# Kernel optimization log

Hardware: AMD Instinct MI355X
Metric: run time of the kernel (lower is better)

The kernel has to match this reference:

```python
import jax, jax.numpy as jnp
import numpy as np

ALPHA = 0.5
N_CACHE = 8
N_HEAD = 16
NUM_MODULES = 4


def _ncn_module(x, xa, W, alpha, n_cache, n_head):
    """One fused NCN module: per-head mix, alpha blend with cache slot (t % n_cache),
    activation, and cache update. x: [B,T,D], xa: [B,n_cache,D], W: [H,dh,dh]."""
    B, T, D = x.shape
    dh = D // n_head
    xh = x.reshape(B, T, n_head, dh).transpose(1, 0, 2, 3)  # [T,B,H,dh]
    cache0 = xa.reshape(B, n_cache, n_head, dh)             # [B,C,H,dh]
    slots = jnp.arange(T) % n_cache                          # cache slot per step

    def step(cache, inp):
        xt, s = inp                                          # xt: [B,H,dh]
        mix = jnp.einsum('bhd,hde->bhe', xt, W)              # per-head mixing
        y = jnp.tanh(alpha * cache[:, s] + (1.0 - alpha) * mix)
        return cache.at[:, s].set(y), y

    cache_f, ys = jax.lax.scan(step, cache0, (xh, slots))
    yi = ys.transpose(1, 0, 2, 3).reshape(B, T, D)
    ya = cache_f.reshape(B, n_cache, D)
    return yi, ya


def setup_inputs() -> dict:
    key = jax.random.key(0)
    k1, k2, k3 = jax.random.split(key, 3)
    B, T, D = 8, 4096, 1024
    dh = D // N_HEAD
    x = jax.random.normal(k1, (B, T, D), dtype=jnp.float32)
    xa = jax.random.normal(k2, (B, N_CACHE, D), dtype=jnp.float32)
    # scale weights for stable tanh recurrence
    weights = jax.random.normal(k3, (NUM_MODULES, N_HEAD, dh, dh), dtype=jnp.float32) / np.sqrt(dh)
    return {"x": x, "xa": xa, "weights": weights}


def reference(x, xa, weights):
    for m in range(NUM_MODULES):
        x, xa = _ncn_module(x, xa, weights[m], ALPHA, N_CACHE, N_HEAD)
    return x, xa
```

## Files before the change

kernel.cpp:

```cpp
#include <hip/hip_runtime.h>
#include <hip/hip_fp16.h>


typedef _Float16 f16;
typedef _Float16 half8 __attribute__((ext_vector_type(8)));
typedef _Float16 half4v __attribute__((ext_vector_type(4)));
typedef float f32x4 __attribute__((ext_vector_type(4)));
typedef unsigned uint4v __attribute__((ext_vector_type(4)));

constexpr int B = 8, T = 4096, D = 1024, H = 16, DH = 64, NC = 8, NM = 4;
constexpr int CH = 256;
constexpr int NCHUNK = T / CH;
constexpr int RPC = 128;

__global__ __launch_bounds__(256, 1)
void ncn_main(const float* __restrict__ x, const float* __restrict__ xa,
              const float* __restrict__ w, float* __restrict__ out) {
  __shared__ __align__(16) unsigned char YL[RPC * 128];
  __shared__ __align__(16) unsigned char MX[64 * 256];

  const int tid = threadIdx.x, lane = tid & 63, wv = tid >> 6;
  const int bx = blockIdx.x;
  const int chalf = bx & 1, h = (bx >> 1) & 15, b = bx >> 5;
  const int cbase = chalf * 4;
  const int lr = lane & 15, lg = lane >> 4;
  const int c = cbase + wv;
  const int d = lane;

  unsigned char* const rows = (unsigned char*)out + (size_t)b * T * 4096;
  const unsigned char* const xrows =
      (const unsigned char*)x + (size_t)b * T * 4096;

  float cache = xa[((size_t)b * NC + c) * D + h * DH + d];

  uint4v pf[8];

  for (int m = 0; m < NM; ++m) {
    const float* wh = w + ((size_t)m * H + h) * DH * DH;
    half8 Wf[4][2];
#pragma unroll
    for (int it = 0; it < 4; ++it)
#pragma unroll
      for (int kt = 0; kt < 2; ++kt)
#pragma unroll
        for (int j = 0; j < 8; ++j)
          Wf[it][kt][j] =
              (f16)wh[(size_t)(kt * 32 + lg * 8 + j) * DH + it * 16 + lr];

    asm volatile("s_waitcnt vmcnt(0)" ::: "memory");
    __syncthreads();

    if (m == 0) {
#pragma unroll
      for (int i = 0; i < 8; ++i) {
        const int gid = i * 256 + tid;
        const int c16 = gid & 15, lt = gid >> 4;
        const int t = ((lt >> 2) << 3) + cbase + (lt & 3);
        pf[i] = *(const uint4v*)(xrows + (size_t)t * 4096 + h * 256 + c16 * 16);
      }
    } else {
#pragma unroll
      for (int i = 0; i < 4; ++i) {
        const int gid = i * 256 + tid;
        const int c16 = gid & 7, lt = gid >> 3;
        const int t = ((lt >> 2) << 3) + cbase + (lt & 3);
        pf[i] = *(const uint4v*)(rows + (size_t)t * 4096 + h * 128 + c16 * 16);
      }
    }

    for (int ch = 0; ch < NCHUNK; ++ch) {
      const int t0 = ch * CH;

      if (m == 0) {
#pragma unroll
        for (int i = 0; i < 8; ++i) {
          const int gid = i * 256 + tid;
          const int c16 = gid & 15, lt = gid >> 4;
          const f32x4 v = __builtin_bit_cast(f32x4, pf[i]);
          half4v hv;
#pragma unroll
          for (int e = 0; e < 4; ++e) hv[e] = (f16)v[e];
          *(half4v*)(YL + lt * 128 + ((c16 * 8) ^ ((lt & 7) << 4))) = hv;
        }
      } else {
#pragma unroll
        for (int i = 0; i < 4; ++i) {
          const int gid = i * 256 + tid;
          const int c16 = gid & 7, lt = gid >> 3;
          *(uint4v*)(YL + lt * 128 + ((c16 * 16) ^ ((lt & 7) << 4))) = pf[i];
        }
      }
      __syncthreads();

      if (ch + 1 < NCHUNK) {
        const int t1 = t0 + CH;
        if (m == 0) {
#pragma unroll
          for (int i = 0; i < 8; ++i) {
            const int gid = i * 256 + tid;
            const int c16 = gid & 15, lt = gid >> 4;
            const int t = t1 + ((lt >> 2) << 3) + cbase + (lt & 3);
            pf[i] = *(const uint4v*)(xrows + (size_t)t * 4096 + h * 256 + c16 * 16);
          }
        } else {
#pragma unroll
          for (int i = 0; i < 4; ++i) {
            const int gid = i * 256 + tid;
            const int c16 = gid & 7, lt = gid >> 3;
            const int t = t1 + ((lt >> 2) << 3) + cbase + (lt & 3);
            pf[i] = *(const uint4v*)(rows + (size_t)t * 4096 + h * 128 + c16 * 16);
          }
        }
      }

#pragma unroll
      for (int q = 0; q < 2; ++q) {
        const int tt = wv * 2 + q;
        const int r = tt * 16 + lr;
        half8 Xf[2];
#pragma unroll
        for (int kt = 0; kt < 2; ++kt)
          Xf[kt] = *(const half8*)(YL + r * 128 +
                                   ((kt * 64 + lg * 16) ^ ((r & 7) << 4)));
        f32x4 acc[4];
#pragma unroll
        for (int it = 0; it < 4; ++it) acc[it] = (f32x4){0.f, 0.f, 0.f, 0.f};
#pragma unroll
        for (int kt = 0; kt < 2; ++kt)
#pragma unroll
          for (int it = 0; it < 4; ++it)
            acc[it] = __builtin_amdgcn_mfma_f32_16x16x32_f16(
                Xf[kt], Wf[it][kt], acc[it], 0, 0, 0);
#pragma unroll
        for (int it = 0; it < 4; ++it) {
          const int e = it * 16 + lr;
#pragma unroll
          for (int j = 0; j < 4; ++j)
            *(f16*)(MX + e * 256 +
                    ((j * 64 + (tt * 4 + lg) * 2) ^ ((e & 7) << 4))) =
                (f16)acc[it][j];
        }
      }
      __syncthreads();

      half8 mxr[4];
#pragma unroll
      for (int k16 = 0; k16 < 4; ++k16)
        mxr[k16] = *(const half8*)(MX + d * 256 +
                                   ((wv * 64 + k16 * 16) ^ ((d & 7) << 4)));
      unsigned char* sp = rows + (size_t)(t0 + c) * 4096 + h * 128 + 2 * d;
#pragma unroll
      for (int k = 0; k < 32; ++k) {
        const float mixv = (float)mxr[k >> 3][k & 7];
        const float z = cache + mixv;
        const float E = __expf(z);
        cache = 1.0f - 2.0f * __builtin_amdgcn_rcpf(E + 1.0f);
        *(__half*)sp = __float2half_rn(cache);
        sp += 8 * 4096;
      }
    }
  }

  float* ya = out + (size_t)B * T * D;
  ya[((size_t)b * NC + c) * D + h * DH + d] = cache;
}

__global__ __launch_bounds__(256)
void expand(float* __restrict__ buf) {
  __shared__ __align__(16) f16 rs[4 * 1024];
  const int tid = threadIdx.x;
  unsigned char* const base = (unsigned char*)buf + (size_t)blockIdx.x * 4 * 4096;
#pragma unroll
  for (int p = 0; p < 2; ++p) {
    const int gid = p * 256 + tid;
    const int row = gid >> 7, c16 = gid & 127;
    *(uint4v*)((unsigned char*)rs + row * 2048 + c16 * 16) =
        *(const uint4v*)(base + (size_t)row * 4096 + c16 * 16);
  }
  __syncthreads();
#pragma unroll
  for (int p = 0; p < 4; ++p) {
    const int gid = p * 256 + tid;
    const int row = gid >> 8, c4 = gid & 255;
    const half4v hv = *(const half4v*)((unsigned char*)rs + row * 2048 + c4 * 8);
    f32x4 v;
#pragma unroll
    for (int e = 0; e < 4; ++e) v[e] = (float)hv[e];
    *(f32x4*)(base + (size_t)row * 4096 + c4 * 16) = v;
  }
}

extern "C" void kernel_launch(void* const* d_in, const int* in_sizes, int n_in,
                              void* d_out, int out_size, void* d_ws, size_t ws_size,
                              hipStream_t stream) {
  (void)in_sizes; (void)n_in; (void)d_ws; (void)ws_size; (void)out_size;
  const float* x  = (const float*)d_in[0];
  const float* xa = (const float*)d_in[1];
  const float* w  = (const float*)d_in[2];
  float* out = (float*)d_out;

  hipLaunchKernelGGL(ncn_main, dim3(256), dim3(256), 0, stream, x, xa, w, out);
  hipLaunchKernelGGL(expand, dim3(B * T / 4), dim3(256), 0, stream, out);
}
```

Measured before the change: 165.3 us.

## Double-buffer chunk GEMM against scan and write final fp32 output directly

Splits the per-chunk work into stage, GEMM issue, GEMM scatter and scan phases, and double-buffers the LDS tiles so the MFMA mixing for the next chunk runs alongside the serial tanh scan of the current one, with one barrier per chunk instead of two. Intermediate fp16 activations go to a compact workspace buffer when one is available. The last module then writes fp32 output directly, which drops the separate expand kernel launch and its extra pass over memory. In exchange it uses twice the shared memory and more registers (mixf array, double accumulators), and it depends on workspace size to take the fast path.

```diff
diff --git a/kernel.cpp b/kernel.cpp
--- a/kernel.cpp
+++ b/kernel.cpp
@@ -11,33 +11,151 @@
 constexpr int B = 8, T = 4096, D = 1024, H = 16, DH = 64, NC = 8, NM = 4;
 constexpr int CH = 256;
 constexpr int NCHUNK = T / CH;
-constexpr int RPC = 128;
-
+constexpr int YLSZ = 128 * 128;
+constexpr int MXSZ = 64 * 256;
+constexpr size_t YWS_BYTES = (size_t)B * T * 2048;
+
+template <bool YWS>
 __global__ __launch_bounds__(256, 1)
 void ncn_main(const float* __restrict__ x, const float* __restrict__ xa,
-              const float* __restrict__ w, float* __restrict__ out) {
-  __shared__ __align__(16) unsigned char YL[RPC * 128];
-  __shared__ __align__(16) unsigned char MX[64 * 256];
+              const float* __restrict__ w, float* __restrict__ out,
+              unsigned char* __restrict__ ybuf) {
+  constexpr int YROW = YWS ? 2048 : 4096;
+  __shared__ __align__(16) unsigned char YL[2 * YLSZ];
+  __shared__ __align__(16) unsigned char MX[2 * MXSZ];
 
   const int tid = threadIdx.x, lane = tid & 63, wv = tid >> 6;
   const int bx = blockIdx.x;
   const int chalf = bx & 1, h = (bx >> 1) & 15, b = bx >> 5;
   const int cbase = chalf * 4;
   const int lr = lane & 15, lg = lane >> 4;
-  const int c = cbase + wv;
-  const int d = lane;
+  const int c = cbase + wv, d = lane;
 
   unsigned char* const rows = (unsigned char*)out + (size_t)b * T * 4096;
   const unsigned char* const xrows =
       (const unsigned char*)x + (size_t)b * T * 4096;
+  unsigned char* const ybase = ybuf + (size_t)b * T * YROW;
 
   float cache = xa[((size_t)b * NC + c) * D + h * DH + d];
 
   uint4v pf[8];
+  half8 Wf[4][2];
+  float mixf[32];
+
+  auto prefetch = [&](int m, int t1) {
+    if (m == 0) {
+#pragma unroll
+      for (int i = 0; i < 8; ++i) {
+        const int gid = i * 256 + tid;
+        const int c16 = gid & 15, lt = gid >> 4;
+        const int t = t1 + ((lt >> 2) << 3) + cbase + (lt & 3);
+        pf[i] = *(const uint4v*)(xrows + (size_t)t * 4096 + h * 256 + c16 * 16);
+      }
+    } else {
+#pragma unroll
+      for (int i = 0; i < 4; ++i) {
+        const int gid = i * 256 + tid;
+        const int c16 = gid & 7, lt = gid >> 3;
+        const int t = t1 + ((lt >> 2) << 3) + cbase + (lt & 3);
+        pf[i] = *(const uint4v*)(ybase + (size_t)t * YROW + h * 128 + c16 * 16);
+      }
+    }
+  };
+  auto stage = [&](int m, int buf) {
+    unsigned char* yb = YL + buf * YLSZ;
+    if (m == 0) {
+#pragma unroll
+      for (int i = 0; i < 8; ++i) {
+        const int gid = i * 256 + tid;
+        const int c16 = gid & 15, lt = gid >> 4;
+        const f32x4 v = __builtin_bit_cast(f32x4, pf[i]);
+        half4v hv;
+#pragma unroll
+        for (int e = 0; e < 4; ++e) hv[e] = (f16)v[e];
+        *(half4v*)(yb + lt * 128 + ((c16 * 8) ^ ((lt & 7) << 4))) = hv;
+      }
+    } else {
+#pragma unroll
+      for (int i = 0; i < 4; ++i) {
+        const int gid = i * 256 + tid;
+        const int c16 = gid & 7, lt = gid >> 3;
+        *(uint4v*)(yb + lt * 128 + ((c16 * 16) ^ ((lt & 7) << 4))) = pf[i];
+      }
+    }
+  };
+  auto gemm_issue = [&](int buf, f32x4 (&acc)[2][4]) {
+    const unsigned char* yb = YL + buf * YLSZ;
+#pragma unroll
+    for (int q = 0; q < 2; ++q) {
+      const int tt = wv * 2 + q;
+      const int r = tt * 16 + lr;
+      half8 Xf[2];
+#pragma unroll
+      for (int kt = 0; kt < 2; ++kt)
+        Xf[kt] = *(const half8*)(yb + r * 128 +
+                                 ((kt * 64 + lg * 16) ^ ((r & 7) << 4)));
+#pragma unroll
+      for (int it = 0; it < 4; ++it) acc[q][it] = (f32x4){0.f, 0.f, 0.f, 0.f};
+#pragma unroll
+      for (int kt = 0; kt < 2; ++kt)
+#pragma unroll
+        for (int it = 0; it < 4; ++it)
+          acc[q][it] = __builtin_amdgcn_mfma_f32_16x16x32_f16(
+              Xf[kt], Wf[it][kt], acc[q][it], 0, 0, 0);
+    }
+  };
+  auto gemm_scatter = [&](int buf, const f32x4 (&acc)[2][4]) {
+    unsigned char* mb = MX + buf * MXSZ;
+#pragma unroll
+    for (int q = 0; q < 2; ++q) {
+      const int tt = wv * 2 + q;
+#pragma unroll
+      for (int it = 0; it < 4; ++it) {
+        const int e = it * 16 + lr;
+#pragma unroll
+        for (int j = 0; j < 4; ++j)
+          *(f16*)(mb + e * 256 +
+                  ((j * 64 + (tt * 4 + lg) * 2) ^ ((e & 7) << 4))) =
+              (f16)acc[q][it][j];
+      }
+    }
+  };
+  auto scan_load = [&](int buf) {
+    const unsigned char* mb = MX + buf * MXSZ;
+    half8 mxr[4];
+#pragma unroll
+    for (int k16 = 0; k16 < 4; ++k16)
+      mxr[k16] = *(const half8*)(mb + d * 256 +
+                                 ((wv * 64 + k16 * 16) ^ ((d & 7) << 4)));
+#pragma unroll
+    for (int k = 0; k < 32; ++k) mixf[k] = (float)mxr[k >> 3][k & 7];
+  };
+  auto scan_run = [&](int m, int t0) {
+    if (m < 3 || !YWS) {
+      unsigned char* sp = ybase + (size_t)(t0 + c) * YROW + h * 128 + 2 * d;
+#pragma unroll
+      for (int k = 0; k < 32; ++k) {
+        const float z = cache + mixf[k];
+        const float E = __expf(z);
+        cache = fmaf(-2.0f, __builtin_amdgcn_rcpf(E + 1.0f), 1.0f);
+        *(__half*)sp = __float2half_rn(cache);
+        sp += 8 * YROW;
+      }
+    } else {
+      unsigned char* sp = rows + (size_t)(t0 + c) * 4096 + h * 256 + 4 * d;
+#pragma unroll
+      for (int k = 0; k < 32; ++k) {
+        const float z = cache + mixf[k];
+        const float E = __expf(z);
+        cache = fmaf(-2.0f, __builtin_amdgcn_rcpf(E + 1.0f), 1.0f);
+        *(float*)sp = cache;
+        sp += 8 * 4096;
+      }
+    }
+  };
 
   for (int m = 0; m < NM; ++m) {
     const float* wh = w + ((size_t)m * H + h) * DH * DH;
-    half8 Wf[4][2];
 #pragma unroll
     for (int it = 0; it < 4; ++it)
 #pragma unroll
@@ -50,114 +168,29 @@
     asm volatile("s_waitcnt vmcnt(0)" ::: "memory");
     __syncthreads();
 
-    if (m == 0) {
-#pragma unroll
-      for (int i = 0; i < 8; ++i) {
-        const int gid = i * 256 + tid;
-        const int c16 = gid & 15, lt = gid >> 4;
-        const int t = ((lt >> 2) << 3) + cbase + (lt & 3);
-        pf[i] = *(const uint4v*)(xrows + (size_t)t * 4096 + h * 256 + c16 * 16);
-      }
-    } else {
-#pragma unroll
-      for (int i = 0; i < 4; ++i) {
-        const int gid = i * 256 + tid;
-        const int c16 = gid & 7, lt = gid >> 3;
-        const int t = ((lt >> 2) << 3) + cbase + (lt & 3);
-        pf[i] = *(const uint4v*)(rows + (size_t)t * 4096 + h * 128 + c16 * 16);
-      }
-    }
+    prefetch(m, 0);
+    stage(m, 0);
+    prefetch(m, CH);
+    __syncthreads();
+    {
+      f32x4 acc0[2][4];
+      gemm_issue(0, acc0);
+      gemm_scatter(0, acc0);
+    }
+    stage(m, 1);
+    prefetch(m, 2 * CH);
+    __syncthreads();
 
     for (int ch = 0; ch < NCHUNK; ++ch) {
-      const int t0 = ch * CH;
-
-      if (m == 0) {
-#pragma unroll
-        for (int i = 0; i < 8; ++i) {
-          const int gid = i * 256 + tid;
-          const int c16 = gid & 15, lt = gid >> 4;
-          const f32x4 v = __builtin_bit_cast(f32x4, pf[i]);
-          half4v hv;
-#pragma unroll
-          for (int e = 0; e < 4; ++e) hv[e] = (f16)v[e];
-          *(half4v*)(YL + lt * 128 + ((c16 * 8) ^ ((lt & 7) << 4))) = hv;
-        }
-      } else {
-#pragma unroll
-        for (int i = 0; i < 4; ++i) {
-          const int gid = i * 256 + tid;
-          const int c16 = gid & 7, lt = gid >> 3;
-          *(uint4v*)(YL + lt * 128 + ((c16 * 16) ^ ((lt & 7) << 4))) = pf[i];
-        }
-      }
+      const int cb = ch & 1;
+      scan_load(cb);
+      f32x4 acc[2][4];
+      if (ch + 1 < NCHUNK) gemm_issue(cb ^ 1, acc);
+      scan_run(m, ch * CH);
+      if (ch + 1 < NCHUNK) gemm_scatter(cb ^ 1, acc);
+      if (ch + 2 < NCHUNK) stage(m, cb);
+      if (ch + 3 < NCHUNK) prefetch(m, (ch + 3) * CH);
       __syncthreads();
-
-      if (ch + 1 < NCHUNK) {
-        const int t1 = t0 + CH;
-        if (m == 0) {
-#pragma unroll
-          for (int i = 0; i < 8; ++i) {
-            const int gid = i * 256 + tid;
-            const int c16 = gid & 15, lt = gid >> 4;
-            const int t = t1 + ((lt >> 2) << 3) + cbase + (lt & 3);
-            pf[i] = *(const uint4v*)(xrows + (size_t)t * 4096 + h * 256 + c16 * 16);
-          }
-        } else {
-#pragma unroll
-          for (int i = 0; i < 4; ++i) {
-            const int gid = i * 256 + tid;
-            const int c16 = gid & 7, lt = gid >> 3;
-            const int t = t1 + ((lt >> 2) << 3) + cbase + (lt & 3);
-            pf[i] = *(const uint4v*)(rows + (size_t)t * 4096 + h * 128 + c16 * 16);
-          }
-        }
-      }
-
-#pragma unroll
-      for (int q = 0; q < 2; ++q) {
-        const int tt = wv * 2 + q;
-        const int r = tt * 16 + lr;
-        half8 Xf[2];
-#pragma unroll
-        for (int kt = 0; kt < 2; ++kt)
-          Xf[kt] = *(const half8*)(YL + r * 128 +
-                                   ((kt * 64 + lg * 16) ^ ((r & 7) << 4)));
-        f32x4 acc[4];
-#pragma unroll
-        for (int it = 0; it < 4; ++it) acc[it] = (f32x4){0.f, 0.f, 0.f, 0.f};
-#pragma unroll
-        for (int kt = 0; kt < 2; ++kt)
-#pragma unroll
-          for (int it = 0; it < 4; ++it)
-            acc[it] = __builtin_amdgcn_mfma_f32_16x16x32_f16(
-                Xf[kt], Wf[it][kt], acc[it], 0, 0, 0);
-#pragma unroll
-        for (int it = 0; it < 4; ++it) {
-          const int e = it * 16 + lr;
-#pragma unroll
-          for (int j = 0; j < 4; ++j)
-            *(f16*)(MX + e * 256 +
-                    ((j * 64 + (tt * 4 + lg) * 2) ^ ((e & 7) << 4))) =
-                (f16)acc[it][j];
-        }
-      }
-      __syncthreads();
-
-      half8 mxr[4];
-#pragma unroll
-      for (int k16 = 0; k16 < 4; ++k16)
-        mxr[k16] = *(const half8*)(MX + d * 256 +
-                                   ((wv * 64 + k16 * 16) ^ ((d & 7) << 4)));
-      unsigned char* sp = rows + (size_t)(t0 + c) * 4096 + h * 128 + 2 * d;
-#pragma unroll
-      for (int k = 0; k < 32; ++k) {
-        const float mixv = (float)mxr[k >> 3][k & 7];
-        const float z = cache + mixv;
-        const float E = __expf(z);
-        cache = 1.0f - 2.0f * __builtin_amdgcn_rcpf(E + 1.0f);
-        *(__half*)sp = __float2half_rn(cache);
-        sp += 8 * 4096;
-      }
     }
   }
 
@@ -193,12 +226,19 @@
 extern "C" void kernel_launch(void* const* d_in, const int* in_sizes, int n_in,
                               void* d_out, int out_size, void* d_ws, size_t ws_size,
                               hipStream_t stream) {
-  (void)in_sizes; (void)n_in; (void)d_ws; (void)ws_size; (void)out_size;
+  (void)in_sizes; (void)n_in; (void)out_size;
   const float* x  = (const float*)d_in[0];
   const float* xa = (const float*)d_in[1];
   const float* w  = (const float*)d_in[2];
   float* out = (float*)d_out;
 
-  hipLaunchKernelGGL(ncn_main, dim3(256), dim3(256), 0, stream, x, xa, w, out);
-  hipLaunchKernelGGL(expand, dim3(B * T / 4), dim3(256), 0, stream, out);
+  const bool usews = (d_ws != nullptr) && (ws_size >= YWS_BYTES);
+  if (usews) {
+    hipLaunchKernelGGL((ncn_main<true>), dim3(256), dim3(256), 0, stream,
+                       x, xa, w, out, (unsigned char*)d_ws);
+  } else {
+    hipLaunchKernelGGL((ncn_main<false>), dim3(256), dim3(256), 0, stream,
+                       x, xa, w, out, (unsigned char*)out);
+    hipLaunchKernelGGL(expand, dim3(B * T / 4), dim3(256), 0, stream, out);
+  }
 }
```

Measured after the change: 180.9 us. +9.5%, slower.

## Make each wave own one cache slot independently, removing block barriers and expand pass

Applied to the files above, without the earlier changes.

Each wave now handles a single (batch, head, slot) recurrence with its own LDS staging and mix buffers, so the per-chunk __syncthreads are replaced by wave-local lgkmcnt waits and a two-deep register prefetch. When a workspace is available, the fp16 intermediate activations for modules 0-2 go to the workspace and the last module writes fp32 straight into the output, which removes the separate expand kernel. The tanh is rewritten to use v_exp_f32 in the base-2 domain, with the log2(e) scaling folded into the carried state. This adds a workspace dependency and smaller per-wave chunks, which may reduce MFMA efficiency per chunk.

```diff
diff --git a/kernel.cpp b/kernel.cpp
--- a/kernel.cpp
+++ b/kernel.cpp
@@ -9,35 +9,85 @@
 typedef unsigned uint4v __attribute__((ext_vector_type(4)));
 
 constexpr int B = 8, T = 4096, D = 1024, H = 16, DH = 64, NC = 8, NM = 4;
-constexpr int CH = 256;
-constexpr int NCHUNK = T / CH;
-constexpr int RPC = 128;
-
+constexpr int KS = 32;
+constexpr int NCH = (T / NC) / KS;
+constexpr size_t YWS_BYTES = (size_t)B * T * 2048;
+constexpr float L2E = 1.44269504088896340736f;
+
+__device__ __forceinline__ float exp2_fast(float v) {
+  float r;
+  asm("v_exp_f32 %0, %1" : "=v"(r) : "v"(v));
+  return r;
+}
+
+template <bool WS>
 __global__ __launch_bounds__(256, 1)
-void ncn_main(const float* __restrict__ x, const float* __restrict__ xa,
-              const float* __restrict__ w, float* __restrict__ out) {
-  __shared__ __align__(16) unsigned char YL[RPC * 128];
-  __shared__ __align__(16) unsigned char MX[64 * 256];
+void ncn_wave(const float* __restrict__ x, const float* __restrict__ xa,
+              const float* __restrict__ w, float* __restrict__ out,
+              unsigned char* __restrict__ ybuf) {
+  constexpr int YROW = WS ? 2048 : 4096;
+  __shared__ __align__(16) unsigned char YST[4][4096];
+  __shared__ __align__(16) unsigned char MXS[4][8192];
 
   const int tid = threadIdx.x, lane = tid & 63, wv = tid >> 6;
-  const int bx = blockIdx.x;
-  const int chalf = bx & 1, h = (bx >> 1) & 15, b = bx >> 5;
-  const int cbase = chalf * 4;
+  const int g = blockIdx.x * 4 + wv;
+  const int c = g & 7, h = (g >> 3) & 15, b = g >> 7;
   const int lr = lane & 15, lg = lane >> 4;
-  const int c = cbase + wv;
-  const int d = lane;
-
-  unsigned char* const rows = (unsigned char*)out + (size_t)b * T * 4096;
-  const unsigned char* const xrows =
-      (const unsigned char*)x + (size_t)b * T * 4096;
-
-  float cache = xa[((size_t)b * NC + c) * D + h * DH + d];
+
+  unsigned char* const yst = YST[wv];
+  unsigned char* const mxs = MXS[wv];
+  const unsigned char* const xb = (const unsigned char*)x + (size_t)b * T * 4096;
+  unsigned char* const ob = (unsigned char*)out + (size_t)b * T * 4096;
+  unsigned char* const yb = ybuf + (size_t)b * T * YROW;
+
+  float y = xa[((size_t)b * NC + c) * D + h * DH + lane];
+  float u = y * L2E;
 
   uint4v pf[8];
+  half8 Wf[4][2];
+
+  auto prefetch = [&](int m, int ch) {
+    const int J0 = ch * KS;
+    if (m == 0) {
+#pragma unroll
+      for (int i = 0; i < 8; ++i) {
+        const int lt = i * 4 + (lane >> 4);
+        const int t = (J0 + lt) * 8 + c;
+        pf[i] = *(const uint4v*)(xb + (size_t)t * 4096 + h * 256 + (lane & 15) * 16);
+      }
+    } else {
+#pragma unroll
+      for (int i = 0; i < 4; ++i) {
+        const int lt = i * 8 + (lane >> 3);
+        const int t = (J0 + lt) * 8 + c;
+        pf[i] = *(const uint4v*)(yb + (size_t)t * YROW + h * 128 + (lane & 7) * 16);
+      }
+    }
+  };
+  auto stage = [&](int m) {
+    if (m == 0) {
+#pragma unroll
+      for (int i = 0; i < 8; ++i) {
+        const int lt = i * 4 + (lane >> 4);
+        const f32x4 v = __builtin_bit_cast(f32x4, pf[i]);
+        const __half2 p0 = __floats2half2_rn(v.x, v.y);
+        const __half2 p1 = __floats2half2_rn(v.z, v.w);
+        uint2 pk;
+        pk.x = __builtin_bit_cast(unsigned, p0);
+        pk.y = __builtin_bit_cast(unsigned, p1);
+        *(uint2*)(yst + lt * 128 + (((lane & 15) * 8) ^ ((lt & 7) << 4))) = pk;
+      }
+    } else {
+#pragma unroll
+      for (int i = 0; i < 4; ++i) {
+        const int lt = i * 8 + (lane >> 3);
+        *(uint4v*)(yst + lt * 128 + (((lane & 7) * 16) ^ ((lt & 7) << 4))) = pf[i];
+      }
+    }
+  };
 
   for (int m = 0; m < NM; ++m) {
     const float* wh = w + ((size_t)m * H + h) * DH * DH;
-    half8 Wf[4][2];
 #pragma unroll
     for (int it = 0; it < 4; ++it)
 #pragma unroll
@@ -48,121 +98,89 @@
               (f16)wh[(size_t)(kt * 32 + lg * 8 + j) * DH + it * 16 + lr];
 
     asm volatile("s_waitcnt vmcnt(0)" ::: "memory");
-    __syncthreads();
-
-    if (m == 0) {
-#pragma unroll
-      for (int i = 0; i < 8; ++i) {
-        const int gid = i * 256 + tid;
-        const int c16 = gid & 15, lt = gid >> 4;
-        const int t = ((lt >> 2) << 3) + cbase + (lt & 3);
-        pf[i] = *(const uint4v*)(xrows + (size_t)t * 4096 + h * 256 + c16 * 16);
-      }
-    } else {
-#pragma unroll
-      for (int i = 0; i < 4; ++i) {
-        const int gid = i * 256 + tid;
-        const int c16 = gid & 7, lt = gid >> 3;
-        const int t = ((lt >> 2) << 3) + cbase + (lt & 3);
-        pf[i] = *(const uint4v*)(rows + (size_t)t * 4096 + h * 128 + c16 * 16);
-      }
-    }
-
-    for (int ch = 0; ch < NCHUNK; ++ch) {
-      const int t0 = ch * CH;
-
-      if (m == 0) {
-#pragma unroll
-        for (int i = 0; i < 8; ++i) {
-          const int gid = i * 256 + tid;
-          const int c16 = gid & 15, lt = gid >> 4;
-          const f32x4 v = __builtin_bit_cast(f32x4, pf[i]);
-          half4v hv;
-#pragma unroll
-          for (int e = 0; e < 4; ++e) hv[e] = (f16)v[e];
-          *(half4v*)(YL + lt * 128 + ((c16 * 8) ^ ((lt & 7) << 4))) = hv;
-        }
-      } else {
-#pragma unroll
-        for (int i = 0; i < 4; ++i) {
-          const int gid = i * 256 + tid;
-          const int c16 = gid & 7, lt = gid >> 3;
-          *(uint4v*)(YL + lt * 128 + ((c16 * 16) ^ ((lt & 7) << 4))) = pf[i];
-        }
-      }
-      __syncthreads();
-
-      if (ch + 1 < NCHUNK) {
-        const int t1 = t0 + CH;
-        if (m == 0) {
-#pragma unroll
-          for (int i = 0; i < 8; ++i) {
-            const int gid = i * 256 + tid;
-            const int c16 = gid & 15, lt = gid >> 4;
-            const int t = t1 + ((lt >> 2) << 3) + cbase + (lt & 3);
-            pf[i] = *(const uint4v*)(xrows + (size_t)t * 4096 + h * 256 + c16 * 16);
-          }
-        } else {
-#pragma unroll
-          for (int i = 0; i < 4; ++i) {
-            const int gid = i * 256 + tid;
-            const int c16 = gid & 7, lt = gid >> 3;
-            const int t = t1 + ((lt >> 2) << 3) + cbase + (lt & 3);
-            pf[i] = *(const uint4v*)(rows + (size_t)t * 4096 + h * 128 + c16 * 16);
-          }
-        }
-      }
-
-#pragma unroll
-      for (int q = 0; q < 2; ++q) {
-        const int tt = wv * 2 + q;
-        const int r = tt * 16 + lr;
+
+    prefetch(m, 0);
+    stage(m);
+    prefetch(m, 1);
+
+    for (int ch = 0; ch < NCH; ++ch) {
+      f32x4 acc[2][4];
+#pragma unroll
+      for (int tq = 0; tq < 2; ++tq) {
         half8 Xf[2];
 #pragma unroll
+        for (int kt = 0; kt < 2; ++kt) {
+          const int lt = tq * 16 + lr;
+          Xf[kt] = *(const half8*)(yst + lt * 128 +
+                                   ((kt * 64 + lg * 16) ^ ((lt & 7) << 4)));
+        }
+#pragma unroll
+        for (int it = 0; it < 4; ++it) acc[tq][it] = (f32x4){0.f, 0.f, 0.f, 0.f};
+#pragma unroll
         for (int kt = 0; kt < 2; ++kt)
-          Xf[kt] = *(const half8*)(YL + r * 128 +
-                                   ((kt * 64 + lg * 16) ^ ((r & 7) << 4)));
-        f32x4 acc[4];
-#pragma unroll
-        for (int it = 0; it < 4; ++it) acc[it] = (f32x4){0.f, 0.f, 0.f, 0.f};
-#pragma unroll
-        for (int kt = 0; kt < 2; ++kt)
 #pragma unroll
           for (int it = 0; it < 4; ++it)
-            acc[it] = __builtin_amdgcn_mfma_f32_16x16x32_f16(
-                Xf[kt], Wf[it][kt], acc[it], 0, 0, 0);
+            acc[tq][it] = __builtin_amdgcn_mfma_f32_16x16x32_f16(
+                Xf[kt], Wf[it][kt], acc[tq][it], 0, 0, 0);
+      }
+      asm volatile("s_waitcnt lgkmcnt(0)" ::: "memory");
+      if (ch + 1 < NCH) stage(m);
+      if (ch + 2 < NCH) prefetch(m, ch + 2);
+
+#pragma unroll
+      for (int tq = 0; tq < 2; ++tq)
 #pragma unroll
         for (int it = 0; it < 4; ++it) {
           const int e = it * 16 + lr;
-#pragma unroll
-          for (int j = 0; j < 4; ++j)
-            *(f16*)(MX + e * 256 +
-                    ((j * 64 + (tt * 4 + lg) * 2) ^ ((e & 7) << 4))) =
-                (f16)acc[it][j];
-        }
-      }
-      __syncthreads();
+          const __half2 p0 = __floats2half2_rn(acc[tq][it].x, acc[tq][it].y);
+          const __half2 p1 = __floats2half2_rn(acc[tq][it].z, acc[tq][it].w);
+          uint2 pk;
+          pk.x = __builtin_bit_cast(unsigned, p0);
+          pk.y = __builtin_bit_cast(unsigned, p1);
+          *(uint2*)(mxs + e * 128 + ((tq * 32 + lg * 8) ^ ((e & 7) << 4))) = pk;
+        }
+      asm volatile("s_waitcnt lgkmcnt(0)" ::: "memory");
 
       half8 mxr[4];
 #pragma unroll
       for (int k16 = 0; k16 < 4; ++k16)
-        mxr[k16] = *(const half8*)(MX + d * 256 +
-                                   ((wv * 64 + k16 * 16) ^ ((d & 7) << 4)));
-      unsigned char* sp = rows + (size_t)(t0 + c) * 4096 + h * 128 + 2 * d;
-#pragma unroll
-      for (int k = 0; k < 32; ++k) {
-        const float mixv = (float)mxr[k >> 3][k & 7];
-        const float z = cache + mixv;
-        const float E = __expf(z);
-        cache = 1.0f - 2.0f * __builtin_amdgcn_rcpf(E + 1.0f);
-        *(__half*)sp = __float2half_rn(cache);
-        sp += 8 * 4096;
+        mxr[k16] = *(const half8*)(mxs + lane * 128 +
+                                   ((k16 * 16) ^ ((lane & 7) << 4)));
+      float mix2[KS];
+#pragma unroll
+      for (int k = 0; k < KS; ++k) mix2[k] = (float)mxr[k >> 3][k & 7] * L2E;
+
+      const int t0 = ch * KS * 8 + c;
+      if (m < 3 || !WS) {
+        unsigned char* sp = yb + (size_t)t0 * YROW + h * 128 + 2 * lane;
+#pragma unroll
+        for (int k = 0; k < KS; ++k) {
+          const float z = u + mix2[k];
+          const float E = exp2_fast(z);
+          const float r = __builtin_amdgcn_rcpf(E + 1.0f);
+          y = fmaf(r, -2.0f, 1.0f);
+          u = fmaf(r, -2.0f * L2E, L2E);
+          *(__half*)sp = __float2half_rn(y);
+          sp += (size_t)8 * YROW;
+        }
+      } else {
+        unsigned char* sp = ob + (size_t)t0 * 4096 + h * 256 + 4 * lane;
+#pragma unroll
+        for (int k = 0; k < KS; ++k) {
+          const float z = u + mix2[k];
+          const float E = exp2_fast(z);
+          const float r = __builtin_amdgcn_rcpf(E + 1.0f);
+          y = fmaf(r, -2.0f, 1.0f);
+          u = fmaf(r, -2.0f * L2E, L2E);
+          *(float*)sp = y;
+          sp += (size_t)8 * 4096;
+        }
       }
     }
   }
 
   float* ya = out + (size_t)B * T * D;
-  ya[((size_t)b * NC + c) * D + h * DH + d] = cache;
+  ya[((size_t)b * NC + c) * D + h * DH + lane] = y;
 }
 
 __global__ __launch_bounds__(256)
@@ -193,12 +211,19 @@
 extern "C" void kernel_launch(void* const* d_in, const int* in_sizes, int n_in,
                               void* d_out, int out_size, void* d_ws, size_t ws_size,
                               hipStream_t stream) {
-  (void)in_sizes; (void)n_in; (void)d_ws; (void)ws_size; (void)out_size;
+  (void)in_sizes; (void)n_in; (void)out_size;
   const float* x  = (const float*)d_in[0];
   const float* xa = (const float*)d_in[1];
   const float* w  = (const float*)d_in[2];
   float* out = (float*)d_out;
 
-  hipLaunchKernelGGL(ncn_main, dim3(256), dim3(256), 0, stream, x, xa, w, out);
-  hipLaunchKernelGGL(expand, dim3(B * T / 4), dim3(256), 0, stream, out);
-}
+  const bool usews = (d_ws != nullptr) && (ws_size >= YWS_BYTES);
+  if (usews) {
+    hipLaunchKernelGGL((ncn_wave<true>), dim3(256), dim3(256), 0, stream,
+                       x, xa, w, out, (unsigned char*)d_ws);
+  } else {
+    hipLaunchKernelGGL((ncn_wave<false>), dim3(256), dim3(256), 0, stream,
+                       x, xa, w, out, (unsigned char*)out);
+    hipLaunchKernelGGL(expand, dim3(B * T / 4), dim3(256), 0, stream, out);
+  }
+}
```

After: 136.2 us. -17.6%, faster.
